# Kernel optimization log

Measured on AMD Instinct MI355X. Metric: run time of the kernel, lower is better.

The kernel has to match this reference:

```python
import jax, jax.numpy as jnp
import numpy as np

N_EMBD = 384
HEAD_SIZE = 64
B, T = 16, 2048


def setup_inputs() -> dict:
    key = jax.random.key(0)
    ks = jax.random.split(key, 7)
    s = 1.0 / np.sqrt(N_EMBD)
    return {
        "x": jax.random.normal(ks[0], (B, T, N_EMBD), dtype=jnp.float32),
        "Wq": jax.random.uniform(ks[1], (N_EMBD, HEAD_SIZE), jnp.float32, -s, s),
        "bq": jax.random.uniform(ks[2], (HEAD_SIZE,), jnp.float32, -s, s),
        "Wk": jax.random.uniform(ks[3], (N_EMBD, HEAD_SIZE), jnp.float32, -s, s),
        "bk": jax.random.uniform(ks[4], (HEAD_SIZE,), jnp.float32, -s, s),
        "Wv": jax.random.uniform(ks[5], (N_EMBD, HEAD_SIZE), jnp.float32, -s, s),
        "bv": jax.random.uniform(ks[6], (HEAD_SIZE,), jnp.float32, -s, s),
    }


def reference(x, Wq, bq, Wk, bk, Wv, bv):
    # QKV projections: [B,T,C] @ [C,H] -> [B,T,H]
    q = x @ Wq + bq
    k = x @ Wk + bk
    v = x @ Wv + bv
    scale = k.shape[-1] ** (-0.5)
    # NOTE: original forward applies NO causal mask (tril buffer unused).
    scores = jnp.einsum("bqh,bkh->bqk", q, k) * scale  # [B,T,T]
    wmap = jax.nn.softmax(scores, axis=-1)
    # dropout is identity in eval mode
    out = jnp.einsum("bqk,bkh->bqh", wmap, v)  # [B,T,H]
    return out
```

## Files before the change

kernel.cpp:

```cpp
#include <hip/hip_runtime.h>
#include <hip/hip_bf16.h>
#include <cstdint>

typedef unsigned short u16;
typedef __attribute__((ext_vector_type(8))) short short8;
typedef __attribute__((ext_vector_type(4))) short short4v;
typedef __attribute__((ext_vector_type(4))) float f32x4;

#define MFMA16(a, b, c) __builtin_amdgcn_mfma_f32_16x16x32_bf16((a), (b), (c), 0, 0, 0)

constexpr int Bn   = 16;
constexpr int Tn   = 2048;
constexpr int Cn   = 384;
constexpr int Hn   = 64;
constexpr long NTOK = (long)Bn * Tn;
constexpr long NELT = NTOK * Hn;
constexpr int SPLITS = 3;

#define QSCALE 0.18033688011112042f

__device__ __forceinline__ u16 f2bf(float f) {
  union { float f; uint32_t u; } c; c.f = f;
  uint32_t u = c.u;
  return (u16)((u + 0x7fffu + ((u >> 16) & 1u)) >> 16);
}

__device__ __forceinline__ uint32_t pkbf(float a, float b) {
  uint32_t d;
  asm("v_cvt_pk_bf16_f32 %0, %1, %2" : "=v"(d) : "v"(a), "v"(b));
  return d;
}

__device__ __forceinline__ short8 ldx8(const float* p) {
  const float4 f0 = *reinterpret_cast<const float4*>(p);
  const float4 f1 = *reinterpret_cast<const float4*>(p + 4);
  union { short8 s8; uint32_t u[4]; } r;
  r.u[0] = pkbf(f0.x, f0.y); r.u[1] = pkbf(f0.z, f0.w);
  r.u[2] = pkbf(f1.x, f1.y); r.u[3] = pkbf(f1.z, f1.w);
  return r.s8;
}

__device__ __forceinline__ void gl16(const u16* g, const u16* l) {
  __builtin_amdgcn_global_load_lds(
      (const __attribute__((address_space(1))) void*)g,
      (__attribute__((address_space(3))) void*)l, 16, 0, 0);
}

__global__ __launch_bounds__(256) void wtrans(
    const float* __restrict__ Wq, const float* __restrict__ Wk,
    const float* __restrict__ Wv, u16* __restrict__ wtd)
{
  __shared__ u16 tile[64][65];
  const int m  = blockIdx.x / 6;
  const int kc = blockIdx.x % 6;
  const float* W = (m == 0) ? Wq : (m == 1) ? Wk : Wv;
  const int t = threadIdx.x;

  {
    const int kr = t >> 2, seg = t & 3;
    const float* src = W + (size_t)(kc * 64 + kr) * Hn + seg * 16;
    #pragma unroll
    for (int j = 0; j < 4; ++j) {
      const float4 f = *reinterpret_cast<const float4*>(src + j * 4);
      u16* p = &tile[kr][seg * 16 + j * 4];
      p[0] = f2bf(f.x); p[1] = f2bf(f.y); p[2] = f2bf(f.z); p[3] = f2bf(f.w);
    }
  }
  __syncthreads();
  {
    const int hr = t >> 2, seg = t & 3;
    union { short8 s; u16 u[8]; } o0, o1;
    #pragma unroll
    for (int j = 0; j < 8; ++j) o0.u[j] = tile[seg * 16 + j][hr];
    #pragma unroll
    for (int j = 0; j < 8; ++j) o1.u[j] = tile[seg * 16 + 8 + j][hr];
    u16* dst = wtd + ((size_t)m * 64 + hr) * Cn + kc * 64 + seg * 16;
    *reinterpret_cast<short8*>(dst)     = o0.s;
    *reinterpret_cast<short8*>(dst + 8) = o1.s;
  }
}

__global__ __launch_bounds__(256, 2) void qkv_proj(
    const float* __restrict__ x, const u16* __restrict__ wtd,
    const float* __restrict__ bq, const float* __restrict__ bk,
    const float* __restrict__ bv,
    u16* __restrict__ oq, u16* __restrict__ ok, u16* __restrict__ ovt)
{
  __shared__ u16 wbuf[3][3 * 64 * 64];

  const int t    = threadIdx.x;
  const int lane = t & 63;
  const int w    = t >> 6;
  const int l15  = lane & 15;
  const int lh   = lane >> 4;
  const long r0  = (long)blockIdx.x * 64;

  int srcoff[6];
  #pragma unroll
  for (int i = 0; i < 6; ++i) {
    const int g = i * 256 + t;
    const int r = g >> 3, c = g & 7;
    srcoff[i] = r * Cn + ((c ^ (r & 7)) << 3);
  }
  const int ldsb = w * 64 * 8;

  const float* xrow = x + (r0 + w * 16 + l15) * Cn;

  const int cks0 = ((lh)     ^ (l15 & 7)) << 3;
  const int cks1 = ((lh + 4) ^ (l15 & 7)) << 3;

  f32x4 acc[3][4];
  #pragma unroll
  for (int m = 0; m < 3; ++m)
    #pragma unroll
    for (int n = 0; n < 4; ++n) acc[m][n] = f32x4{0.f, 0.f, 0.f, 0.f};

  #pragma unroll
  for (int i = 0; i < 6; ++i)
    gl16(wtd + srcoff[i], &wbuf[0][(i * 256) * 8 + ldsb]);
  short8 aCur0 = ldx8(xrow + lh * 8);
  short8 aCur1 = ldx8(xrow + 32 + lh * 8);
  #pragma unroll
  for (int i = 0; i < 6; ++i)
    gl16(wtd + 64 + srcoff[i], &wbuf[1][(i * 256) * 8 + ldsb]);
  short8 aNx10 = ldx8(xrow + 64 + lh * 8);
  short8 aNx11 = ldx8(xrow + 96 + lh * 8);
  short8 aNx20, aNx21;
  asm volatile("s_waitcnt vmcnt(14)" ::: "memory");
  __builtin_amdgcn_s_barrier();
  __builtin_amdgcn_sched_barrier(0);

  for (int kc = 0; kc < 6; ++kc) {
    const int cb = kc % 3;
    const int sb = (kc + 2) % 3;
    if (kc + 2 < 6) {
      #pragma unroll
      for (int i = 0; i < 6; ++i)
        gl16(wtd + (kc + 2) * 64 + srcoff[i], &wbuf[sb][(i * 256) * 8 + ldsb]);
      const float* p = xrow + (kc + 2) * 64 + lh * 8;
      aNx20 = ldx8(p);
      aNx21 = ldx8(p + 32);
    }

    const u16* wc = &wbuf[cb][0];
    #pragma unroll
    for (int m = 0; m < 3; ++m)
      #pragma unroll
      for (int n = 0; n < 4; ++n) {
        const int row = m * 64 + n * 16 + l15;
        const short8 b0 = *reinterpret_cast<const short8*>(&wc[row * 64 + cks0]);
        acc[m][n] = MFMA16(aCur0, b0, acc[m][n]);
        const short8 b1 = *reinterpret_cast<const short8*>(&wc[row * 64 + cks1]);
        acc[m][n] = MFMA16(aCur1, b1, acc[m][n]);
      }

    if (kc + 1 < 6) {
      if (kc + 2 < 6) asm volatile("s_waitcnt vmcnt(14)" ::: "memory");
      else            asm volatile("s_waitcnt vmcnt(4)"  ::: "memory");
      __builtin_amdgcn_s_barrier();
      __builtin_amdgcn_sched_barrier(0);
      aCur0 = aNx10; aCur1 = aNx11;
      aNx10 = aNx20; aNx11 = aNx21;
    }
  }

  {
    const float* bias[2] = {bq, bk};
    u16*         dst[2]  = {oq, ok};
    const float  scl[2]  = {QSCALE, 1.0f};
    #pragma unroll
    for (int m = 0; m < 2; ++m) {
      #pragma unroll
      for (int n = 0; n < 4; ++n) {
        int col = n * 16 + l15;
        float bb = bias[m][col];
        #pragma unroll
        for (int r = 0; r < 4; ++r) {
          int row = lh * 4 + r;
          dst[m][(r0 + w * 16 + row) * Hn + col] = f2bf((acc[m][n][r] + bb) * scl[m]);
        }
      }
    }
  }
  {
    const long g    = r0 + w * 16 + lh * 4;
    const long bidx = g >> 11;
    const long tloc = g & 2047;
    const int  u    = (int)(tloc & 63);
    const long tb   = tloc & ~63L;
    const int  slotb = 32 * ((u >> 5) & 1) + 8 * ((u >> 2) & 3) + 4 * ((u >> 4) & 1);
    #pragma unroll
    for (int n = 0; n < 4; ++n) {
      int col = n * 16 + l15;
      float bb = bv[col];
      short4v pk;
      #pragma unroll
      for (int r = 0; r < 4; ++r) pk[r] = (short)f2bf(acc[2][n][r] + bb);
      *reinterpret_cast<short4v*>(ovt + (bidx * Hn + col) * Tn + tb + slotb) = pk;
    }
  }
}

__global__ __launch_bounds__(512, 6) void flash_attn(
    const u16* __restrict__ q, const u16* __restrict__ k,
    const u16* __restrict__ vt, float* __restrict__ opart,
    float* __restrict__ lpart)
{
  __shared__ u16 kbuf[3][64 * 64];
  __shared__ u16 vbuf[3][64 * 64];

  const int t    = threadIdx.x;
  const int lane = t & 63;
  const int w    = t >> 6;
  const int l15  = lane & 15;
  const int lh   = lane >> 4;
  const int swz_id = (blockIdx.x & 7) * 96 + (blockIdx.x >> 3);
  const int b     = swz_id / 48;
  const int rsw   = swz_id % 48;
  const int split = rsw / 16;
  const int qt    = rsw % 16;
  const long rowbase = (long)b * Tn + qt * 128;
  const int it0 = (split * 32) / 3;
  const int it1 = ((split + 1) * 32) / 3;

  short8 aq0, aq1;
  {
    const u16* qrow = q + (rowbase + w * 16 + l15) * Hn;
    aq0 = *reinterpret_cast<const short8*>(qrow + lh * 8);
    aq1 = *reinterpret_cast<const short8*>(qrow + 32 + lh * 8);
  }

  union { short8 s8; uint32_t u[4]; } ON;
  #pragma unroll
  for (int i = 0; i < 4; ++i) ON.u[i] = 0x3F803F80u;

  f32x4 o[4];
  #pragma unroll
  for (int m = 0; m < 4; ++m) o[m] = f32x4{0.f, 0.f, 0.f, 0.f};
  f32x4 ls = f32x4{0.f, 0.f, 0.f, 0.f};

  const u16* kb_g = k  + (long)b * Tn * Hn;
  const u16* vb_g = vt + (long)b * Hn * Tn;

  const int rg = t >> 3, cg = t & 7;
  const long ksrc = (long)rg * Hn + ((cg ^ (rg & 7)) << 3);
  const long vsrc = (long)rg * Tn + ((cg ^ (rg & 7)) << 3);
  const int wbase = w * 64 * 8;

  const int swz  = l15 & 7;
  const int cks0 = ((0 * 4 + lh) ^ swz) << 3;
  const int cks1 = ((1 * 4 + lh) ^ swz) << 3;
  const int rfr  = l15 * 64;

  {
    gl16(kb_g + (long)it0 * 64 * Hn + ksrc, &kbuf[0][wbase]);
    gl16(vb_g + it0 * 64 + vsrc,            &vbuf[0][wbase]);
    gl16(kb_g + (long)(it0 + 1) * 64 * Hn + ksrc, &kbuf[1][wbase]);
    gl16(vb_g + (it0 + 1) * 64 + vsrc,            &vbuf[1][wbase]);
  }
  asm volatile("s_waitcnt vmcnt(2)" ::: "memory");
  __builtin_amdgcn_s_barrier();
  __builtin_amdgcn_sched_barrier(0);

  for (int it = it0; it < it1; ++it) {
    const int cb = (it - it0) % 3;
    const int sb = (it - it0 + 2) % 3;
    if (it + 2 < it1) {
      gl16(kb_g + (long)(it + 2) * 64 * Hn + ksrc, &kbuf[sb][wbase]);
      gl16(vb_g + (it + 2) * 64 + vsrc,            &vbuf[sb][wbase]);
    }

    const u16* kc  = &kbuf[cb][0];
    const u16* vcb = &vbuf[cb][0];

    f32x4 s[4];
    #pragma unroll
    for (int n = 0; n < 4; ++n) s[n] = f32x4{0.f, 0.f, 0.f, 0.f};
    #pragma unroll
    for (int n = 0; n < 4; ++n) {
      const short8 ak0 = *reinterpret_cast<const short8*>(&kc[n * 1024 + rfr + cks0]);
      s[n] = MFMA16(ak0, aq0, s[n]);
      const short8 ak1 = *reinterpret_cast<const short8*>(&kc[n * 1024 + rfr + cks1]);
      s[n] = MFMA16(ak1, aq1, s[n]);
    }

    #pragma unroll
    for (int n = 0; n < 4; ++n)
      #pragma unroll
      for (int r = 0; r < 4; ++r)
        s[n][r] = __builtin_amdgcn_exp2f(s[n][r]);

    union { short8 s8; uint32_t u[4]; } B0, B1;
    B0.u[0] = pkbf(s[0][0], s[0][1]); B0.u[1] = pkbf(s[0][2], s[0][3]);
    B0.u[2] = pkbf(s[1][0], s[1][1]); B0.u[3] = pkbf(s[1][2], s[1][3]);
    B1.u[0] = pkbf(s[2][0], s[2][1]); B1.u[1] = pkbf(s[2][2], s[2][3]);
    B1.u[2] = pkbf(s[3][0], s[3][1]); B1.u[3] = pkbf(s[3][2], s[3][3]);

    #pragma unroll
    for (int m = 0; m < 4; ++m) {
      const short8 av0 = *reinterpret_cast<const short8*>(&vcb[m * 1024 + rfr + cks0]);
      o[m] = MFMA16(av0, B0.s8, o[m]);
      const short8 av1 = *reinterpret_cast<const short8*>(&vcb[m * 1024 + rfr + cks1]);
      o[m] = MFMA16(av1, B1.s8, o[m]);
    }
    ls = MFMA16(ON.s8, B0.s8, ls);
    ls = MFMA16(ON.s8, B1.s8, ls);

    if (it + 1 < it1) {
      if (it + 2 < it1) asm volatile("s_waitcnt vmcnt(2)" ::: "memory");
      else              asm volatile("s_waitcnt vmcnt(0)" ::: "memory");
      __builtin_amdgcn_s_barrier();
      __builtin_amdgcn_sched_barrier(0);
    }
  }

  {
    const float tot = ls[0];
    const long qrow = rowbase + w * 16 + l15;
    float* od = opart + ((long)split * NELT) + qrow * Hn;
    #pragma unroll
    for (int m = 0; m < 4; ++m) {
      float4 vv;
      vv.x = o[m][0]; vv.y = o[m][1]; vv.z = o[m][2]; vv.w = o[m][3];
      *reinterpret_cast<float4*>(od + m * 16 + lh * 4) = vv;
    }
    if (lh == 0) lpart[(long)split * NTOK + qrow] = tot;
  }
}

__global__ __launch_bounds__(256) void combine(
    const float* __restrict__ op, const float* __restrict__ lp,
    float* __restrict__ out)
{
  const long idx  = (long)blockIdx.x * 256 + threadIdx.x;
  const long base = idx * 4;
  const long row  = base >> 6;
  float4 acc = *reinterpret_cast<const float4*>(op + base);
  float lsum = lp[row];
  #pragma unroll
  for (int s = 1; s < SPLITS; ++s) {
    const float4 c = *reinterpret_cast<const float4*>(op + s * NELT + base);
    acc.x += c.x; acc.y += c.y; acc.z += c.z; acc.w += c.w;
    lsum += lp[s * NTOK + row];
  }
  const float linv = 1.0f / lsum;
  float4 r;
  r.x = acc.x * linv; r.y = acc.y * linv; r.z = acc.z * linv; r.w = acc.w * linv;
  *reinterpret_cast<float4*>(out + base) = r;
}

extern "C" void kernel_launch(void* const* d_in, const int* in_sizes, int n_in,
                              void* d_out, int out_size, void* d_ws, size_t ws_size,
                              hipStream_t stream) {
  const float* x  = (const float*)d_in[0];
  const float* Wq = (const float*)d_in[1];
  const float* bq = (const float*)d_in[2];
  const float* Wk = (const float*)d_in[3];
  const float* bk = (const float*)d_in[4];
  const float* Wv = (const float*)d_in[5];
  const float* bv = (const float*)d_in[6];
  float* out = (float*)d_out;

  u16* qs  = (u16*)d_ws;
  u16* ks  = qs + NELT;
  u16* vs  = ks + NELT;
  u16* wtd = vs + NELT;
  float* op = (float*)(wtd + 3 * 64 * Cn);
  float* lp = op + (long)SPLITS * NELT;

  hipLaunchKernelGGL(wtrans, dim3(18), dim3(256), 0, stream, Wq, Wk, Wv, wtd);
  hipLaunchKernelGGL(qkv_proj, dim3((int)(NTOK / 64)), dim3(256), 0, stream,
                     x, wtd, bq, bk, bv, qs, ks, vs);
  hipLaunchKernelGGL(flash_attn, dim3(16 * 16 * SPLITS), dim3(512), 0, stream,
                     qs, ks, vs, op, lp);
  hipLaunchKernelGGL(combine, dim3((int)(NELT / 4 / 256)), dim3(256), 0, stream,
                     op, lp, out);
}
```

Before: 55.15 us.

## Use smaller attention blocks with five KV splits and bf16 partial outputs

```diff
diff --git a/kernel.cpp b/kernel.cpp
--- a/kernel.cpp
+++ b/kernel.cpp
@@ -15,7 +15,7 @@
 constexpr int Hn   = 64;
 constexpr long NTOK = (long)Bn * Tn;
 constexpr long NELT = NTOK * Hn;
-constexpr int SPLITS = 3;
+constexpr int SPLITS = 5;
 
 #define QSCALE 0.18033688011112042f
 
@@ -201,27 +201,27 @@
   }
 }
 
-__global__ __launch_bounds__(512, 6) void flash_attn(
+__global__ __launch_bounds__(256, 5) void flash_attn(
     const u16* __restrict__ q, const u16* __restrict__ k,
-    const u16* __restrict__ vt, float* __restrict__ opart,
+    const u16* __restrict__ vt, u16* __restrict__ opart,
     float* __restrict__ lpart)
 {
-  __shared__ u16 kbuf[3][64 * 64];
-  __shared__ u16 vbuf[3][64 * 64];
+  __shared__ u16 kbuf[2][64 * 64];
+  __shared__ u16 vbuf[2][64 * 64];
 
   const int t    = threadIdx.x;
   const int lane = t & 63;
   const int w    = t >> 6;
   const int l15  = lane & 15;
   const int lh   = lane >> 4;
-  const int swz_id = (blockIdx.x & 7) * 96 + (blockIdx.x >> 3);
-  const int b     = swz_id / 48;
-  const int rsw   = swz_id % 48;
-  const int split = rsw / 16;
-  const int qt    = rsw % 16;
-  const long rowbase = (long)b * Tn + qt * 128;
-  const int it0 = (split * 32) / 3;
-  const int it1 = ((split + 1) * 32) / 3;
+  const int swz_id = (blockIdx.x & 7) * 320 + (blockIdx.x >> 3);
+  const int b     = swz_id / 160;
+  const int rem   = swz_id % 160;
+  const int split = rem / 32;
+  const int qt    = rem % 32;
+  const long rowbase = (long)b * Tn + qt * 64;
+  const int it0 = (split * 32) / SPLITS;
+  const int it1 = ((split + 1) * 32) / SPLITS;
 
   short8 aq0, aq1;
   {
@@ -242,10 +242,15 @@
   const u16* kb_g = k  + (long)b * Tn * Hn;
   const u16* vb_g = vt + (long)b * Hn * Tn;
 
-  const int rg = t >> 3, cg = t & 7;
-  const long ksrc = (long)rg * Hn + ((cg ^ (rg & 7)) << 3);
-  const long vsrc = (long)rg * Tn + ((cg ^ (rg & 7)) << 3);
-  const int wbase = w * 64 * 8;
+  const int g0 = t, g1 = 256 + t;
+  const int r0g = g0 >> 3, c0g = g0 & 7;
+  const int r1g = g1 >> 3, c1g = g1 & 7;
+  const long ksrc0 = (long)r0g * Hn + ((c0g ^ (r0g & 7)) << 3);
+  const long ksrc1 = (long)r1g * Hn + ((c1g ^ (r1g & 7)) << 3);
+  const long vsrc0 = (long)r0g * Tn + ((c0g ^ (r0g & 7)) << 3);
+  const long vsrc1 = (long)r1g * Tn + ((c1g ^ (r1g & 7)) << 3);
+  const int wb0 = w * 64 * 8;
+  const int wb1 = wb0 + 256 * 8;
 
   const int swz  = l15 & 7;
   const int cks0 = ((0 * 4 + lh) ^ swz) << 3;
@@ -253,29 +258,35 @@
   const int rfr  = l15 * 64;
 
   {
-    gl16(kb_g + (long)it0 * 64 * Hn + ksrc, &kbuf[0][wbase]);
-    gl16(vb_g + it0 * 64 + vsrc,            &vbuf[0][wbase]);
-    gl16(kb_g + (long)(it0 + 1) * 64 * Hn + ksrc, &kbuf[1][wbase]);
-    gl16(vb_g + (it0 + 1) * 64 + vsrc,            &vbuf[1][wbase]);
-  }
-  asm volatile("s_waitcnt vmcnt(2)" ::: "memory");
+    const u16* kt = kb_g + (long)it0 * 64 * Hn;
+    const u16* vp = vb_g + it0 * 64;
+    gl16(kt + ksrc0, &kbuf[0][wb0]);
+    gl16(kt + ksrc1, &kbuf[0][wb1]);
+    gl16(vp + vsrc0, &vbuf[0][wb0]);
+    gl16(vp + vsrc1, &vbuf[0][wb1]);
+  }
+  asm volatile("s_waitcnt vmcnt(0)" ::: "memory");
   __builtin_amdgcn_s_barrier();
   __builtin_amdgcn_sched_barrier(0);
 
+  int cur = 0;
   for (int it = it0; it < it1; ++it) {
-    const int cb = (it - it0) % 3;
-    const int sb = (it - it0 + 2) % 3;
-    if (it + 2 < it1) {
-      gl16(kb_g + (long)(it + 2) * 64 * Hn + ksrc, &kbuf[sb][wbase]);
-      gl16(vb_g + (it + 2) * 64 + vsrc,            &vbuf[sb][wbase]);
-    }
-
-    const u16* kc  = &kbuf[cb][0];
-    const u16* vcb = &vbuf[cb][0];
+    if (it + 1 < it1) {
+      const u16* kt = kb_g + (long)(it + 1) * 64 * Hn;
+      const u16* vp = vb_g + (it + 1) * 64;
+      gl16(kt + ksrc0, &kbuf[cur ^ 1][wb0]);
+      gl16(kt + ksrc1, &kbuf[cur ^ 1][wb1]);
+      gl16(vp + vsrc0, &vbuf[cur ^ 1][wb0]);
+      gl16(vp + vsrc1, &vbuf[cur ^ 1][wb1]);
+    }
+
+    const u16* kc  = &kbuf[cur][0];
+    const u16* vcb = &vbuf[cur][0];
 
     f32x4 s[4];
     #pragma unroll
     for (int n = 0; n < 4; ++n) s[n] = f32x4{0.f, 0.f, 0.f, 0.f};
+    __builtin_amdgcn_s_setprio(1);
     #pragma unroll
     for (int n = 0; n < 4; ++n) {
       const short8 ak0 = *reinterpret_cast<const short8*>(&kc[n * 1024 + rfr + cks0]);
@@ -283,6 +294,7 @@
       const short8 ak1 = *reinterpret_cast<const short8*>(&kc[n * 1024 + rfr + cks1]);
       s[n] = MFMA16(ak1, aq1, s[n]);
     }
+    __builtin_amdgcn_s_setprio(0);
 
     #pragma unroll
     for (int n = 0; n < 4; ++n)
@@ -296,6 +308,7 @@
     B1.u[0] = pkbf(s[2][0], s[2][1]); B1.u[1] = pkbf(s[2][2], s[2][3]);
     B1.u[2] = pkbf(s[3][0], s[3][1]); B1.u[3] = pkbf(s[3][2], s[3][3]);
 
+    __builtin_amdgcn_s_setprio(1);
     #pragma unroll
     for (int m = 0; m < 4; ++m) {
       const short8 av0 = *reinterpret_cast<const short8*>(&vcb[m * 1024 + rfr + cks0]);
@@ -305,48 +318,59 @@
     }
     ls = MFMA16(ON.s8, B0.s8, ls);
     ls = MFMA16(ON.s8, B1.s8, ls);
+    __builtin_amdgcn_s_setprio(0);
 
     if (it + 1 < it1) {
-      if (it + 2 < it1) asm volatile("s_waitcnt vmcnt(2)" ::: "memory");
-      else              asm volatile("s_waitcnt vmcnt(0)" ::: "memory");
+      asm volatile("s_waitcnt vmcnt(0)" ::: "memory");
       __builtin_amdgcn_s_barrier();
       __builtin_amdgcn_sched_barrier(0);
+      cur ^= 1;
     }
   }
 
   {
     const float tot = ls[0];
     const long qrow = rowbase + w * 16 + l15;
-    float* od = opart + ((long)split * NELT) + qrow * Hn;
+    u16* od = opart + ((long)split * NELT) + qrow * Hn;
     #pragma unroll
     for (int m = 0; m < 4; ++m) {
-      float4 vv;
-      vv.x = o[m][0]; vv.y = o[m][1]; vv.z = o[m][2]; vv.w = o[m][3];
-      *reinterpret_cast<float4*>(od + m * 16 + lh * 4) = vv;
+      uint32_t p0 = pkbf(o[m][0], o[m][1]);
+      uint32_t p1 = pkbf(o[m][2], o[m][3]);
+      uint32_t* dst = reinterpret_cast<uint32_t*>(od + m * 16 + lh * 4);
+      dst[0] = p0; dst[1] = p1;
     }
     if (lh == 0) lpart[(long)split * NTOK + qrow] = tot;
   }
 }
 
 __global__ __launch_bounds__(256) void combine(
-    const float* __restrict__ op, const float* __restrict__ lp,
+    const u16* __restrict__ op, const float* __restrict__ lp,
     float* __restrict__ out)
 {
   const long idx  = (long)blockIdx.x * 256 + threadIdx.x;
-  const long base = idx * 4;
+  const long base = idx * 8;
   const long row  = base >> 6;
-  float4 acc = *reinterpret_cast<const float4*>(op + base);
-  float lsum = lp[row];
-  #pragma unroll
-  for (int s = 1; s < SPLITS; ++s) {
-    const float4 c = *reinterpret_cast<const float4*>(op + s * NELT + base);
-    acc.x += c.x; acc.y += c.y; acc.z += c.z; acc.w += c.w;
-    lsum += lp[s * NTOK + row];
-  }
+  float lsum = 0.f;
+  #pragma unroll
+  for (int s = 0; s < SPLITS; ++s) lsum += lp[s * NTOK + row];
   const float linv = 1.0f / lsum;
-  float4 r;
-  r.x = acc.x * linv; r.y = acc.y * linv; r.z = acc.z * linv; r.w = acc.w * linv;
-  *reinterpret_cast<float4*>(out + base) = r;
+
+  float acc[8] = {0.f, 0.f, 0.f, 0.f, 0.f, 0.f, 0.f, 0.f};
+  #pragma unroll
+  for (int s = 0; s < SPLITS; ++s) {
+    union { short8 v; u16 u[8]; } pk;
+    pk.v = *reinterpret_cast<const short8*>(op + s * NELT + base);
+    #pragma unroll
+    for (int j = 0; j < 8; ++j) {
+      union { uint32_t u; float f; } c; c.u = ((uint32_t)pk.u[j]) << 16;
+      acc[j] += c.f;
+    }
+  }
+  float4 r0, r1;
+  r0.x = acc[0] * linv; r0.y = acc[1] * linv; r0.z = acc[2] * linv; r0.w = acc[3] * linv;
+  r1.x = acc[4] * linv; r1.y = acc[5] * linv; r1.z = acc[6] * linv; r1.w = acc[7] * linv;
+  *reinterpret_cast<float4*>(out + base)     = r0;
+  *reinterpret_cast<float4*>(out + base + 4) = r1;
 }
 
 extern "C" void kernel_launch(void* const* d_in, const int* in_sizes, int n_in,
@@ -365,14 +389,14 @@
   u16* ks  = qs + NELT;
   u16* vs  = ks + NELT;
   u16* wtd = vs + NELT;
-  float* op = (float*)(wtd + 3 * 64 * Cn);
-  float* lp = op + (long)SPLITS * NELT;
+  u16* op  = wtd + 3 * 64 * Cn;
+  float* lp = (float*)(op + (long)SPLITS * NELT);
 
   hipLaunchKernelGGL(wtrans, dim3(18), dim3(256), 0, stream, Wq, Wk, Wv, wtd);
   hipLaunchKernelGGL(qkv_proj, dim3((int)(NTOK / 64)), dim3(256), 0, stream,
                      x, wtd, bq, bk, bv, qs, ks, vs);
-  hipLaunchKernelGGL(flash_attn, dim3(16 * 16 * SPLITS), dim3(512), 0, stream,
+  hipLaunchKernelGGL(flash_attn, dim3(16 * 32 * SPLITS), dim3(256), 0, stream,
                      qs, ks, vs, op, lp);
-  hipLaunchKernelGGL(combine, dim3((int)(NELT / 4 / 256)), dim3(256), 0, stream,
+  hipLaunchKernelGGL(combine, dim3((int)(NELT / 8 / 256)), dim3(256), 0, stream,
                      op, lp, out);
 }
```

After: 59.52 us. 7.9% more time.
